# Kernel optimization log

Hardware: AMD Instinct MI355X
Metric: run time of the kernel (lower is better)

The kernel has to match this reference:

```python
import jax, jax.numpy as jnp
import numpy as np

B, S, IN, HID = 128, 512, 1024, 1024
CHI, KAPPA, DT = 0.638, 0.35, 0.01
NC = 6  # num zeta corridors


def setup_inputs() -> dict:
    key = jax.random.key(0)
    ks = jax.random.split(key, 10)
    def rn(k, shp, s=0.02):
        return jax.random.normal(k, shp, dtype=jnp.float32) * s
    return {
        "x": jax.random.normal(ks[0], (B, S, IN), dtype=jnp.float32),
        "W_gates": rn(ks[1], (IN + HID, 4 * HID)),  # fused [i|f|g|o] gate weights
        "b_gates": jnp.zeros((4 * HID,), jnp.float32),
        "mirror_W": rn(ks[2], (HID, HID)),
        "mirror_b": jnp.zeros((HID,), jnp.float32),
        "curv_W1": rn(ks[3], (HID, HID // 2)),
        "curv_b1": jnp.zeros((HID // 2,), jnp.float32),
        "curv_W2": rn(ks[4], (HID // 2, 1)),
        "curv_b2": jnp.zeros((1,), jnp.float32),
        "evo_W": rn(ks[5], (HID, HID)),
        "evo_b": jnp.zeros((HID,), jnp.float32),
        "zeta_w": jax.random.normal(ks[6], (NC,), dtype=jnp.float32),
        "zeta_p": jax.random.normal(ks[7], (NC,), dtype=jnp.float32),
    }


def _zeta_loss(zw, zp):
    # Per recurrent step seq_len==1 so s-points are (sigma=0.5, t=-2) for every batch
    # element; the functional-equation loss is therefore a single scalar independent
    # of the hidden state, and the mean over identical points equals that scalar.
    L = 0.2 + 0.1 * jnp.arange(NC, dtype=jnp.float32)  # corridor lengths
    s0 = jnp.complex64(0.5 - 2.0j)
    def xi(s):
        t1 = jnp.exp(-s * L)
        t2 = jax.nn.sigmoid(zp).astype(jnp.complex64) * jnp.exp(-(1.0 - s) * L)
        return jnp.sum(jax.nn.sigmoid(zw).astype(jnp.complex64) * 0.5 * (t1 + t2))
    d = xi(s0) - xi(1.0 - s0)
    return (d * jnp.conj(d)).real  # |Xi(s) - Xi(1-s)|^2


def reference(x, W_gates, b_gates, mirror_W, mirror_b,
              curv_W1, curv_b1, curv_W2, curv_b2,
              evo_W, evo_b, zeta_w, zeta_p):
    Wx, Wh = W_gates[:IN], W_gates[IN:]
    # Precompute the input contribution of all 4 gates for every timestep (one big GEMM).
    gx = jnp.einsum('bsi,ig->bsg', x, Wx) + b_gates        # [B,S,4H]
    gx = jnp.swapaxes(gx, 0, 1)                            # [S,B,4H] for scan
    h0 = jnp.zeros((x.shape[0], HID), x.dtype)
    c0 = jnp.zeros((x.shape[0], HID), x.dtype)

    def step(carry, g):
        h, c = carry
        gates = g + h @ Wh                                  # [B,4H]
        i, f, gg, o = jnp.split(gates, 4, axis=-1)
        i, f, o = jax.nn.sigmoid(i), jax.nn.sigmoid(f), jax.nn.sigmoid(o)
        gg = jnp.tanh(gg)
        c = f * c + i * gg
        # curvature coupling: scalar curvature per batch element gates an evolution step
        kap = CHI * (jax.nn.relu(c @ curv_W1 + curv_b1) @ curv_W2 + curv_b2)  # [B,1]
        c = c + DT * kap * (c @ evo_W + evo_b)
        # mirror operator + guardian threshold
        h = jnp.tanh((o * jnp.tanh(c)) @ mirror_W + mirror_b)
        h = h / (1.0 + KAPPA * jnp.abs(h))
        return (h, c), h

    (h, c), ys = jax.lax.scan(step, (h0, c0), gx)
    outputs = jnp.swapaxes(ys, 0, 1)                        # [B,S,H]
    # zeta regularization loss is identical each step, so the seq-mean equals one eval
    return outputs, h, c, _zeta_loss(zeta_w, zeta_p)
```

## Files before the change

### kernel.cpp

```cpp
#include <hip/hip_runtime.h>
#include <hip/hip_bf16.h>
#include <math.h>
#include <stdint.h>

#define B_    128
#define S_    512
#define IN_   1024
#define HID_  1024
#define CHI_  0.638f
#define KAPPA_ 0.35f
#define DT_   0.01f
#define CH    32
#define NCHUNK (S_/CH)

#define OUT_H 67108864
#define OUT_C 67239936
#define OUT_Z 67371008

#define WS_CNT   0
#define WS_KP    2048
#define WS_HBF   6144
#define WS_CF32  268288
#define WS_STATE_BYTES 792576
#define WS_CBF   792576
#define WS_MBF   1054720
#define WS_WGT   1316864
#define WS_EVOT  18094080
#define WS_MIRT  20191232
#define WS_C1T   22288384
#define WS_XBF   23336960
#define WS_GXC   31725568

using s16x8 = __attribute__((ext_vector_type(8))) short;
using s16x4 = __attribute__((ext_vector_type(4))) short;
using f32x4 = __attribute__((ext_vector_type(4))) float;
typedef unsigned long long u64;

static __device__ __forceinline__ short f2bf(float x){
  unsigned int u = __float_as_uint(x);
  u = (u + 0x7FFFu + ((u >> 16) & 1u)) >> 16;
  return (short)u;
}
static __device__ __forceinline__ float b2f(short s){
  return __uint_as_float(((unsigned int)(unsigned short)s) << 16);
}
static __device__ __forceinline__ float sigf(float x){
  return 1.f / (1.f + __expf(-x));
}
static __device__ __forceinline__ float tanhf_(float x){
  return 1.f - 2.f / (__expf(2.f * x) + 1.f);
}
static __device__ __forceinline__ f32x4 mfma16(s16x8 a, s16x8 b, f32x4 c){
  return __builtin_amdgcn_mfma_f32_16x16x32_bf16(a, b, c, 0, 0, 0);
}

static __device__ __forceinline__ u64 ld_coh_u64(const void* p){
  return __hip_atomic_load((const u64*)p, __ATOMIC_RELAXED, __HIP_MEMORY_SCOPE_AGENT);
}
static __device__ __forceinline__ void st_coh_u64(void* p, u64 v){
  __hip_atomic_store((u64*)p, v, __ATOMIC_RELAXED, __HIP_MEMORY_SCOPE_AGENT);
}
static __device__ __forceinline__ float ld_coh_f32(const float* p){
  return __hip_atomic_load(p, __ATOMIC_RELAXED, __HIP_MEMORY_SCOPE_AGENT);
}
static __device__ __forceinline__ void st_coh_f32(float* p, float v){
  __hip_atomic_store(p, v, __ATOMIC_RELAXED, __HIP_MEMORY_SCOPE_AGENT);
}
static __device__ __forceinline__ unsigned ld_coh_u32(const unsigned* p){
  return __hip_atomic_load(p, __ATOMIC_RELAXED, __HIP_MEMORY_SCOPE_AGENT);
}
static __device__ __forceinline__ void st_coh_u32(unsigned* p, unsigned v){
  __hip_atomic_store(p, v, __ATOMIC_RELAXED, __HIP_MEMORY_SCOPE_AGENT);
}
static __device__ __forceinline__ void at_add_f32(float* p, float v){
  __hip_atomic_fetch_add(p, v, __ATOMIC_RELAXED, __HIP_MEMORY_SCOPE_AGENT);
}
static __device__ __forceinline__ s16x8 ld_coh16B(const short* p){
  union { u64 q[2]; s16x8 v; } u;
  u.q[0] = ld_coh_u64(p);
  u.q[1] = ld_coh_u64(p + 4);
  return u.v;
}

static __device__ __forceinline__ void gbar(unsigned* arr, int n, unsigned gen){
  asm volatile("s_waitcnt vmcnt(0)" ::: "memory");
  __syncthreads();
  if (threadIdx.x < 32){
    if (threadIdx.x == 0) st_coh_u32(arr + n, gen);
    unsigned v = ld_coh_u32(arr + threadIdx.x);
    while (!__all(v >= gen)){
      __builtin_amdgcn_s_sleep(2);
      v = ld_coh_u32(arr + threadIdx.x);
    }
  }
  __syncthreads();
}

__global__ void transpose_bf(const float* __restrict__ in, short* __restrict__ out,
                             int R, int C){
  __shared__ float tile[32][33];
  int c0 = blockIdx.x * 32, r0 = blockIdx.y * 32;
  int tc = threadIdx.x & 31, tr = threadIdx.x >> 5;
  #pragma unroll
  for (int i = 0; i < 4; i++){
    int r = tr + i * 8;
    tile[r][tc] = in[(size_t)(r0 + r) * C + (c0 + tc)];
  }
  __syncthreads();
  #pragma unroll
  for (int i = 0; i < 4; i++){
    int cc = tr + i * 8;
    out[(size_t)(c0 + cc) * R + (r0 + tc)] = f2bf(tile[tc][cc]);
  }
}

__global__ void conv_x(const float* __restrict__ x, short* __restrict__ xbf, int t0){
  int rb = blockIdx.x;
  int tl = rb >> 7, b = rb & 127;
  const float* src = x + ((size_t)b * S_ + (t0 + tl)) * (size_t)IN_;
  short* dst = xbf + (size_t)rb * IN_;
  int i = threadIdx.x * 4;
  float4 v = *(const float4*)(src + i);
  s16x4 o; o[0]=f2bf(v.x); o[1]=f2bf(v.y); o[2]=f2bf(v.z); o[3]=f2bf(v.w);
  *(s16x4*)(dst + i) = o;
}

__global__ __launch_bounds__(256, 2) void gemm_gx(const short* __restrict__ Ax,
                                                  const short* __restrict__ wgT,
                                                  short* __restrict__ gxc){
  __shared__ short As[128 * 32];
  __shared__ short Bs[128 * 32];
  const int tid = threadIdx.x, w = tid >> 6, l = tid & 63;
  const int wm = w & 1, wn = w >> 1;
  const int bn = blockIdx.x, bm = blockIdx.y;
  const int lc = l & 15, kg = l >> 4;
  f32x4 acc[4][4];
  #pragma unroll
  for (int i = 0; i < 4; i++)
    #pragma unroll
    for (int j = 0; j < 4; j++) acc[i][j] = f32x4{0.f, 0.f, 0.f, 0.f};

  const int srow = tid >> 1;
  const int so = (tid & 1) * 32;
  const short* ga = Ax  + (size_t)(bm * 128 + srow) * 1024 + (so >> 1);
  const short* gb = wgT + (size_t)(bn * 128 + srow) * 2048 + (so >> 1);
  const int sp0 = srow * 64 + ((so)      ^ ((srow & 3) << 4));
  const int sp1 = srow * 64 + ((so + 16) ^ ((srow & 3) << 4));

  uint4 ra0, ra1, rb0, rb1;
  auto LD = [&](int kt){
    ra0 = *(const uint4*)(ga + kt * 32);
    ra1 = *(const uint4*)(ga + kt * 32 + 8);
    rb0 = *(const uint4*)(gb + kt * 32);
    rb1 = *(const uint4*)(gb + kt * 32 + 8);
  };
  LD(0);
  for (int kt = 0; kt < 32; ++kt){
    __syncthreads();
    *(uint4*)((char*)As + sp0) = ra0;
    *(uint4*)((char*)As + sp1) = ra1;
    *(uint4*)((char*)Bs + sp0) = rb0;
    *(uint4*)((char*)Bs + sp1) = rb1;
    __syncthreads();
    if (kt + 1 < 32) LD(kt + 1);
    s16x8 af[4], bfr[4];
    #pragma unroll
    for (int mf = 0; mf < 4; ++mf){
      int row = wm * 64 + mf * 16 + lc;
      af[mf] = *(const s16x8*)((const char*)As + row * 64 + ((kg * 16) ^ ((row & 3) << 4)));
    }
    #pragma unroll
    for (int nf = 0; nf < 4; ++nf){
      int row = wn * 64 + nf * 16 + lc;
      bfr[nf] = *(const s16x8*)((const char*)Bs + row * 64 + ((kg * 16) ^ ((row & 3) << 4)));
    }
    #pragma unroll
    for (int mf = 0; mf < 4; ++mf)
      #pragma unroll
      for (int nf = 0; nf < 4; ++nf)
        acc[mf][nf] = mfma16(af[mf], bfr[nf], acc[mf][nf]);
  }
  #pragma unroll
  for (int mf = 0; mf < 4; ++mf){
    #pragma unroll
    for (int nf = 0; nf < 4; ++nf){
      int gg = wm * 4 + mf;
      int gc = bn * 128 + wn * 64 + nf * 16 + lc;
      s16x4 pk;
      #pragma unroll
      for (int r = 0; r < 4; r++) pk[r] = f2bf(acc[mf][nf][r]);
      *(s16x4*)(gxc + (((size_t)bm * 8 + gg) * 4096 + gc) * 16 + kg * 4) = pk;
    }
  }
}

struct cpx { double r, i; };
static __device__ cpx cexp_(cpx z){ double e = exp(z.r); return {e * cos(z.i), e * sin(z.i)}; }
static __device__ cpx xi_(double sr, double si, const float* zw, const float* zp){
  cpx acc{0.0, 0.0};
  for (int i = 0; i < 6; i++){
    double L = 0.2 + 0.1 * i;
    double sw = 1.0 / (1.0 + exp(-(double)zw[i]));
    double sp = 1.0 / (1.0 + exp(-(double)zp[i]));
    cpx t1 = cexp_({-sr * L, -si * L});
    cpx t2 = cexp_({-(1.0 - sr) * L, si * L});
    acc.r += sw * 0.5 * (t1.r + sp * t2.r);
    acc.i += sw * 0.5 * (t1.i + sp * t2.i);
  }
  return acc;
}
__global__ void zeta_k(const float* __restrict__ zw, const float* __restrict__ zp,
                       float* __restrict__ dz){
  if (threadIdx.x == 0 && blockIdx.x == 0){
    cpx a = xi_(0.5, -2.0, zw, zp);
    cpx b = xi_(0.5,  2.0, zw, zp);
    double dr = a.r - b.r, di = a.i - b.i;
    dz[0] = (float)(dr * dr + di * di);
  }
}

#define RSLOT(slot, j) ((char*)red + (slot) * 8192 + (size_t)l * 128 + (((j) * 16) ^ ((l & 7) << 4)))

__global__ __launch_bounds__(512, 2) void scan_k(
    const short* __restrict__ wgT, const short* __restrict__ evoT,
    const short* __restrict__ mirT, const short* __restrict__ c1T,
    const short* __restrict__ gxc,
    const float* __restrict__ bg,  const float* __restrict__ evob,
    const float* __restrict__ mirb, const float* __restrict__ cb1,
    const float* __restrict__ cw2, const float* __restrict__ cb2,
    short* __restrict__ hbf, short* __restrict__ cbf, short* __restrict__ mbf,
    float* __restrict__ cf32, float* __restrict__ kp,
    unsigned int* __restrict__ cnt, float* __restrict__ dout, int t0)
{
  const int tid = threadIdx.x;
  const int w = tid >> 6, l = tid & 63;
  const int lc = l & 15, kg = l >> 4;
  const int bi = blockIdx.x;
  const int g = bi >> 5, n = bi & 31;
  unsigned* arr = cnt + g * 64;

  __shared__ float red[4][64][32];
  __shared__ float gatesL[4][16][33];
  __shared__ float eL[16][33];
  __shared__ float kpart[16][8];
  __shared__ float kapL[16];
  __shared__ short stL[16][32];
  __shared__ float hfL[16][32];

  const short* hG = hbf + (size_t)g * 16384;
  const short* cG = cbf + (size_t)g * 16384;
  const short* mG = mbf + (size_t)g * 16384;
  float* kpg = kp + g * 128;

  const int pl = (tid & 127) >> 1, ph = tid & 1;
  const size_t poff = (size_t)(n * 64 + pl) * 8 + ph * 4;
  const int psr = pl & 15, psc = (pl >> 4) * 8 + ph * 4;

  const int orow = tid >> 5, ocolL = tid & 31;
  const int ocol = n * 32 + ocolL;
  const size_t oidx = (size_t)(g * 16 + orow) * HID_ + ocol;
  float c_state = cf32[oidx];
  float o_reg = 0.f;
  float bgv[4];
  #pragma unroll
  for (int q = 0; q < 4; q++) bgv[q] = bg[q * 1024 + ocol];
  const float cb2v = cb2[0];

  const short* bqp[4][2];
  #pragma unroll
  for (int q = 0; q < 4; q++)
    #pragma unroll
    for (int cf = 0; cf < 2; cf++)
      bqp[q][cf] = wgT + (size_t)(q * 1024 + n * 32 + cf * 16 + lc) * 2048 + 1024 + w * 128 + kg * 8;
  const short* bevo0 = evoT + (size_t)(n * 32 + lc) * 1024 + w * 128 + kg * 8;
  const short* bevo1 = bevo0 + 16 * 1024;
  const short* bcur  = c1T + (size_t)(n * 16 + lc) * 1024 + w * 128 + kg * 8;
  const short* bmir0 = mirT + (size_t)(n * 32 + lc) * 1024 + w * 128 + kg * 8;
  const short* bmir1 = bmir0 + 16 * 1024;
  const float eb0 = evob[n * 32 + lc], eb1 = evob[n * 32 + 16 + lc];
  const float c1bv = cb1[n * 16 + lc], c2wv = cw2[n * 16 + lc];
  const float mb0 = mirb[n * 32 + lc], mb1 = mirb[n * 32 + 16 + lc];

  unsigned gen = (unsigned)t0 * 4;

  for (int lt = 0; lt < CH; ++lt){
    const int t = t0 + lt;

    float gxv[4];
    #pragma unroll
    for (int q = 0; q < 4; q++)
      gxv[q] = b2f(gxc[(((size_t)lt * 8 + g) * 4096 + q * 1024 + ocol) * 16 + orow]);

    {
      f32x4 acc[4][2];
      #pragma unroll
      for (int q = 0; q < 4; q++){ acc[q][0] = f32x4{0,0,0,0}; acc[q][1] = f32x4{0,0,0,0}; }
      #pragma unroll
      for (int ks = 0; ks < 4; ++ks){
        int kq = w * 4 + ks;
        s16x8 a = ld_coh16B(hG + (size_t)(kq * 64 + l) * 8);
        #pragma unroll
        for (int q = 0; q < 4; q++){
          s16x8 b0 = *(const s16x8*)(bqp[q][0] + ks * 32);
          s16x8 b1 = *(const s16x8*)(bqp[q][1] + ks * 32);
          acc[q][0] = mfma16(a, b0, acc[q][0]);
          acc[q][1] = mfma16(a, b1, acc[q][1]);
        }
      }
      f32x4* accf = (f32x4*)acc;
      if (w >= 4){
        #pragma unroll
        for (int j = 0; j < 8; j++) *(f32x4*)RSLOT(w - 4, j) = accf[j];
      }
      __syncthreads();
      if (w < 4){
        #pragma unroll
        for (int j = 0; j < 8; j++) accf[j] += *(const f32x4*)RSLOT(w, j);
      }
      __syncthreads();
      if (w == 2 || w == 3){
        #pragma unroll
        for (int j = 0; j < 8; j++) *(f32x4*)RSLOT(w - 2, j) = accf[j];
      }
      __syncthreads();
      if (w < 2){
        #pragma unroll
        for (int j = 0; j < 8; j++) accf[j] += *(const f32x4*)RSLOT(w, j);
      }
      __syncthreads();
      if (w == 1){
        #pragma unroll
        for (int j = 0; j < 8; j++) *(f32x4*)RSLOT(0, j) = accf[j];
      }
      __syncthreads();
      if (w == 0){
        #pragma unroll
        for (int j = 0; j < 8; j++) accf[j] += *(const f32x4*)RSLOT(0, j);
        #pragma unroll
        for (int q = 0; q < 4; q++)
          #pragma unroll
          for (int cf = 0; cf < 2; cf++)
            #pragma unroll
            for (int r = 0; r < 4; r++)
              gatesL[q][kg * 4 + r][cf * 16 + lc] = acc[q][cf][r];
      }
      __syncthreads();
      float pre[4];
      #pragma unroll
      for (int q = 0; q < 4; q++)
        pre[q] = gatesL[q][orow][ocolL] + bgv[q] + gxv[q];
      float ii = sigf(pre[0]), ff = sigf(pre[1]);
      float gt = tanhf_(pre[2]);
      o_reg = sigf(pre[3]);
      c_state = ff * c_state + ii * gt;
      stL[orow][ocolL] = f2bf(c_state);
      __syncthreads();
      if (tid < 128)
        st_coh_u64((void*)(cG + poff), *(const u64*)&stL[psr][psc]);
    }
    gbar(arr, n, ++gen);

    {
      f32x4 e0{0,0,0,0}, e1{0,0,0,0}, cv{0,0,0,0};
      #pragma unroll
      for (int ks = 0; ks < 4; ++ks){
        int kq = w * 4 + ks;
        s16x8 a = ld_coh16B(cG + (size_t)(kq * 64 + l) * 8);
        s16x8 b0 = *(const s16x8*)(bevo0 + ks * 32);
        s16x8 b1 = *(const s16x8*)(bevo1 + ks * 32);
        s16x8 bc = *(const s16x8*)(bcur + ks * 32);
        e0 = mfma16(a, b0, e0);
        e1 = mfma16(a, b1, e1);
        cv = mfma16(a, bc, cv);
      }
      if (w >= 4){
        *(f32x4*)RSLOT(w - 4, 0) = e0; *(f32x4*)RSLOT(w - 4, 1) = e1; *(f32x4*)RSLOT(w - 4, 2) = cv;
      }
      __syncthreads();
      if (w < 4){
        e0 += *(const f32x4*)RSLOT(w, 0); e1 += *(const f32x4*)RSLOT(w, 1); cv += *(const f32x4*)RSLOT(w, 2);
      }
      __syncthreads();
      if (w == 2 || w == 3){
        *(f32x4*)RSLOT(w - 2, 0) = e0; *(f32x4*)RSLOT(w - 2, 1) = e1; *(f32x4*)RSLOT(w - 2, 2) = cv;
      }
      __syncthreads();
      if (w < 2){
        e0 += *(const f32x4*)RSLOT(w, 0); e1 += *(const f32x4*)RSLOT(w, 1); cv += *(const f32x4*)RSLOT(w, 2);
      }
      __syncthreads();
      if (w == 1){
        *(f32x4*)RSLOT(0, 0) = e0; *(f32x4*)RSLOT(0, 1) = e1; *(f32x4*)RSLOT(0, 2) = cv;
      }
      __syncthreads();
      if (w == 0){
        e0 += *(const f32x4*)RSLOT(0, 0); e1 += *(const f32x4*)RSLOT(0, 1); cv += *(const f32x4*)RSLOT(0, 2);
        #pragma unroll
        for (int r = 0; r < 4; r++){
          eL[kg * 4 + r][lc]      = e0[r] + eb0;
          eL[kg * 4 + r][16 + lc] = e1[r] + eb1;
          float v = fmaxf(cv[r] + c1bv, 0.f) * c2wv;
          v += __shfl_xor(v, 1); v += __shfl_xor(v, 2);
          v += __shfl_xor(v, 4); v += __shfl_xor(v, 8);
          if (lc == 0)
            at_add_f32(kpg + (kg * 4 + r) * 8 + (n >> 2), v);
        }
      }
    }
    gbar(arr, n, ++gen);

    {
      if (tid < 128)
        kpart[tid >> 3][tid & 7] = ld_coh_f32(kpg + tid);
      __syncthreads();
      if (tid < 16){
        float s = 0.f;
        #pragma unroll
        for (int j = 0; j < 8; j++) s += kpart[tid][j];
        kapL[tid] = CHI_ * (s + cb2v);
      }
      __syncthreads();
      {
        float e = eL[orow][ocolL];
        c_state = c_state + DT_ * kapL[orow] * e;
        float mm = o_reg * tanhf_(c_state);
        stL[orow][ocolL] = f2bf(mm);
        if (t == S_ - 1) dout[OUT_C + oidx] = c_state;
        if (lt == CH - 1) cf32[oidx] = c_state;
      }
      __syncthreads();
      if (tid < 128)
        st_coh_u64((void*)(mG + poff), *(const u64*)&stL[psr][psc]);
    }
    gbar(arr, n, ++gen);

    {
      f32x4 h0{0,0,0,0}, h1{0,0,0,0};
      #pragma unroll
      for (int ks = 0; ks < 4; ++ks){
        int kq = w * 4 + ks;
        s16x8 a = ld_coh16B(mG + (size_t)(kq * 64 + l) * 8);
        s16x8 b0 = *(const s16x8*)(bmir0 + ks * 32);
        s16x8 b1 = *(const s16x8*)(bmir1 + ks * 32);
        h0 = mfma16(a, b0, h0);
        h1 = mfma16(a, b1, h1);
      }
      if (w >= 4){ *(f32x4*)RSLOT(w - 4, 0) = h0; *(f32x4*)RSLOT(w - 4, 1) = h1; }
      __syncthreads();
      if (w < 4){ h0 += *(const f32x4*)RSLOT(w, 0); h1 += *(const f32x4*)RSLOT(w, 1); }
      __syncthreads();
      if (w == 2 || w == 3){ *(f32x4*)RSLOT(w - 2, 0) = h0; *(f32x4*)RSLOT(w - 2, 1) = h1; }
      __syncthreads();
      if (w < 2){ h0 += *(const f32x4*)RSLOT(w, 0); h1 += *(const f32x4*)RSLOT(w, 1); }
      __syncthreads();
      if (w == 1){ *(f32x4*)RSLOT(0, 0) = h0; *(f32x4*)RSLOT(0, 1) = h1; }
      __syncthreads();
      if (w == 0){
        h0 += *(const f32x4*)RSLOT(0, 0); h1 += *(const f32x4*)RSLOT(0, 1);
        #pragma unroll
        for (int cf = 0; cf < 2; cf++){
          #pragma unroll
          for (int r = 0; r < 4; r++){
            int row = kg * 4 + r;
            float hv = tanhf_((cf ? h1[r] : h0[r]) + (cf ? mb1 : mb0));
            hv = hv / (1.f + KAPPA_ * fabsf(hv));
            hfL[row][cf * 16 + lc] = hv;
            stL[row][cf * 16 + lc] = f2bf(hv);
          }
        }
      }
      __syncthreads();
      {
        float hv = hfL[orow][ocolL];
        dout[(size_t)(g * 16 + orow) * 524288 + (size_t)t * 1024 + ocol] = hv;
        if (t == S_ - 1) dout[OUT_H + oidx] = hv;
      }
      if (tid < 128)
        st_coh_u64((void*)(hG + poff), *(const u64*)&stL[psr][psc]);
      if (n == 0 && tid >= 128 && tid < 256)
        st_coh_f32(kpg + (tid - 128), 0.f);
    }
    gbar(arr, n, ++gen);
  }
}

extern "C" void kernel_launch(void* const* d_in, const int* in_sizes, int n_in,
                              void* d_out, int out_size, void* d_ws, size_t ws_size,
                              hipStream_t stream)
{
  (void)in_sizes; (void)n_in; (void)out_size; (void)ws_size;
  const float* x   = (const float*)d_in[0];
  const float* Wg  = (const float*)d_in[1];
  const float* bg  = (const float*)d_in[2];
  const float* miW = (const float*)d_in[3];
  const float* mib = (const float*)d_in[4];
  const float* c1W = (const float*)d_in[5];
  const float* c1b = (const float*)d_in[6];
  const float* c2W = (const float*)d_in[7];
  const float* c2b = (const float*)d_in[8];
  const float* evW = (const float*)d_in[9];
  const float* evb = (const float*)d_in[10];
  const float* zw  = (const float*)d_in[11];
  const float* zp  = (const float*)d_in[12];
  float* out = (float*)d_out;
  char* ws = (char*)d_ws;

  unsigned int* cnt = (unsigned int*)(ws + WS_CNT);
  float* kpb  = (float*)(ws + WS_KP);
  short* hbf  = (short*)(ws + WS_HBF);
  float* cf32 = (float*)(ws + WS_CF32);
  short* cbf  = (short*)(ws + WS_CBF);
  short* mbf  = (short*)(ws + WS_MBF);
  short* wgT  = (short*)(ws + WS_WGT);
  short* evoT = (short*)(ws + WS_EVOT);
  short* mirT = (short*)(ws + WS_MIRT);
  short* c1T  = (short*)(ws + WS_C1T);
  short* xbf  = (short*)(ws + WS_XBF);
  short* gxc  = (short*)(ws + WS_GXC);

  hipMemsetAsync(ws, 0, WS_STATE_BYTES, stream);

  transpose_bf<<<dim3(4096/32, 2048/32), 256, 0, stream>>>(Wg,  wgT, 2048, 4096);
  transpose_bf<<<dim3(1024/32, 1024/32), 256, 0, stream>>>(evW, evoT, 1024, 1024);
  transpose_bf<<<dim3(1024/32, 1024/32), 256, 0, stream>>>(miW, mirT, 1024, 1024);
  transpose_bf<<<dim3(512/32, 1024/32),  256, 0, stream>>>(c1W, c1T, 1024, 512);

  zeta_k<<<1, 64, 0, stream>>>(zw, zp, out + OUT_Z);

  for (int ch = 0; ch < NCHUNK; ++ch){
    conv_x<<<dim3(CH * 128), 256, 0, stream>>>(x, xbf, ch * CH);
    gemm_gx<<<dim3(32, CH), 256, 0, stream>>>(xbf, wgT, gxc);
    scan_k<<<dim3(256), 512, 0, stream>>>(wgT, evoT, mirT, c1T, gxc,
                                          bg, evb, mib, c1b, c2W, c2b,
                                          hbf, cbf, mbf, cf32, kpb,
                                          cnt, out, ch * CH);
  }
}
```

Baseline: 11.95 ms.

## Stage shared A operand in LDS and split waves by output tile instead of K

Each recurrent phase now loads the full 16x1024 bf16 activation tile for the group into LDS once, using coherent global loads, and then has each wave compute a distinct output tile across the whole K dimension. This replaces the earlier K-split across 8 waves, which needed a multi-round LDS tree reduction with several __syncthreads per phase. The change removes those reduction barriers and the per-wave coherent A loads. In exchange, the evo/curv and mirror phases use only 2-3 of the 8 waves, each running a longer serial MFMA chain, so latency on the critical path may rise.

```diff
diff --git a/kernel.cpp b/kernel.cpp
--- a/kernel.cpp
+++ b/kernel.cpp
@@ -74,12 +74,6 @@
 }
 static __device__ __forceinline__ void at_add_f32(float* p, float v){
   __hip_atomic_fetch_add(p, v, __ATOMIC_RELAXED, __HIP_MEMORY_SCOPE_AGENT);
-}
-static __device__ __forceinline__ s16x8 ld_coh16B(const short* p){
-  union { u64 q[2]; s16x8 v; } u;
-  u.q[0] = ld_coh_u64(p);
-  u.q[1] = ld_coh_u64(p + 4);
-  return u.v;
 }
 
 static __device__ __forceinline__ void gbar(unsigned* arr, int n, unsigned gen){
@@ -219,8 +213,6 @@
   }
 }
 
-#define RSLOT(slot, j) ((char*)red + (slot) * 8192 + (size_t)l * 128 + (((j) * 16) ^ ((l & 7) << 4)))
-
 __global__ __launch_bounds__(512, 2) void scan_k(
     const short* __restrict__ wgT, const short* __restrict__ evoT,
     const short* __restrict__ mirT, const short* __restrict__ c1T,
@@ -239,7 +231,7 @@
   const int g = bi >> 5, n = bi & 31;
   unsigned* arr = cnt + g * 64;
 
-  __shared__ float red[4][64][32];
+  __shared__ short aS[16384];
   __shared__ float gatesL[4][16][33];
   __shared__ float eL[16][33];
   __shared__ float kpart[16][8];
@@ -251,6 +243,24 @@
   const short* cG = cbf + (size_t)g * 16384;
   const short* mG = mbf + (size_t)g * 16384;
   float* kpg = kp + g * 128;
+
+  auto stage = [&](const short* G){
+    const short* p = G + tid * 8;
+    s16x8 v0, v1, v2, v3;
+    asm volatile(
+      "global_load_dwordx4 %0, %4, off sc0 sc1\n\t"
+      "global_load_dwordx4 %1, %5, off sc0 sc1\n\t"
+      "global_load_dwordx4 %2, %6, off sc0 sc1\n\t"
+      "global_load_dwordx4 %3, %7, off sc0 sc1\n\t"
+      "s_waitcnt vmcnt(0)"
+      : "=&v"(v0), "=&v"(v1), "=&v"(v2), "=&v"(v3)
+      : "v"(p), "v"(p + 4096), "v"(p + 8192), "v"(p + 12288)
+      : "memory");
+    *(s16x8*)(aS + tid * 8)         = v0;
+    *(s16x8*)(aS + tid * 8 + 4096)  = v1;
+    *(s16x8*)(aS + tid * 8 + 8192)  = v2;
+    *(s16x8*)(aS + tid * 8 + 12288) = v3;
+  };
 
   const int pl = (tid & 127) >> 1, ph = tid & 1;
   const size_t poff = (size_t)(n * 64 + pl) * 8 + ph * 4;
@@ -266,20 +276,12 @@
   for (int q = 0; q < 4; q++) bgv[q] = bg[q * 1024 + ocol];
   const float cb2v = cb2[0];
 
-  const short* bqp[4][2];
-  #pragma unroll
-  for (int q = 0; q < 4; q++)
-    #pragma unroll
-    for (int cf = 0; cf < 2; cf++)
-      bqp[q][cf] = wgT + (size_t)(q * 1024 + n * 32 + cf * 16 + lc) * 2048 + 1024 + w * 128 + kg * 8;
-  const short* bevo0 = evoT + (size_t)(n * 32 + lc) * 1024 + w * 128 + kg * 8;
-  const short* bevo1 = bevo0 + 16 * 1024;
-  const short* bcur  = c1T + (size_t)(n * 16 + lc) * 1024 + w * 128 + kg * 8;
-  const short* bmir0 = mirT + (size_t)(n * 32 + lc) * 1024 + w * 128 + kg * 8;
-  const short* bmir1 = bmir0 + 16 * 1024;
-  const float eb0 = evob[n * 32 + lc], eb1 = evob[n * 32 + 16 + lc];
+  const int qA = w >> 1, cfA = w & 1;
+  const short* bA = wgT + (size_t)(qA * 1024 + n * 32 + cfA * 16 + lc) * 2048 + 1024 + kg * 8;
+  const short* bB = evoT + (size_t)(n * 32 + (w & 1) * 16 + lc) * 1024 + kg * 8;
+  const short* bC = c1T + (size_t)(n * 16 + lc) * 1024 + kg * 8;
+  const short* bD = mirT + (size_t)(n * 32 + (w & 1) * 16 + lc) * 1024 + kg * 8;
   const float c1bv = cb1[n * 16 + lc], c2wv = cw2[n * 16 + lc];
-  const float mb0 = mirb[n * 32 + lc], mb1 = mirb[n * 32 + 16 + lc];
 
   unsigned gen = (unsigned)t0 * 4;
 
@@ -292,58 +294,18 @@
       gxv[q] = b2f(gxc[(((size_t)lt * 8 + g) * 4096 + q * 1024 + ocol) * 16 + orow]);
 
     {
-      f32x4 acc[4][2];
+      stage(hG);
+      __syncthreads();
+      f32x4 acc{0.f, 0.f, 0.f, 0.f};
       #pragma unroll
-      for (int q = 0; q < 4; q++){ acc[q][0] = f32x4{0,0,0,0}; acc[q][1] = f32x4{0,0,0,0}; }
+      for (int kq = 0; kq < 32; ++kq){
+        s16x8 a = *(const s16x8*)(aS + (kq * 64 + l) * 8);
+        s16x8 b = *(const s16x8*)(bA + kq * 32);
+        acc = mfma16(a, b, acc);
+      }
       #pragma unroll
-      for (int ks = 0; ks < 4; ++ks){
-        int kq = w * 4 + ks;
-        s16x8 a = ld_coh16B(hG + (size_t)(kq * 64 + l) * 8);
-        #pragma unroll
-        for (int q = 0; q < 4; q++){
-          s16x8 b0 = *(const s16x8*)(bqp[q][0] + ks * 32);
-          s16x8 b1 = *(const s16x8*)(bqp[q][1] + ks * 32);
-          acc[q][0] = mfma16(a, b0, acc[q][0]);
-          acc[q][1] = mfma16(a, b1, acc[q][1]);
-        }
-      }
-      f32x4* accf = (f32x4*)acc;
-      if (w >= 4){
-        #pragma unroll
-        for (int j = 0; j < 8; j++) *(f32x4*)RSLOT(w - 4, j) = accf[j];
-      }
-      __syncthreads();
-      if (w < 4){
-        #pragma unroll
-        for (int j = 0; j < 8; j++) accf[j] += *(const f32x4*)RSLOT(w, j);
-      }
-      __syncthreads();
-      if (w == 2 || w == 3){
-        #pragma unroll
-        for (int j = 0; j < 8; j++) *(f32x4*)RSLOT(w - 2, j) = accf[j];
-      }
-      __syncthreads();
-      if (w < 2){
-        #pragma unroll
-        for (int j = 0; j < 8; j++) accf[j] += *(const f32x4*)RSLOT(w, j);
-      }
-      __syncthreads();
-      if (w == 1){
-        #pragma unroll
-        for (int j = 0; j < 8; j++) *(f32x4*)RSLOT(0, j) = accf[j];
-      }
-      __syncthreads();
-      if (w == 0){
-        #pragma unroll
-        for (int j = 0; j < 8; j++) accf[j] += *(const f32x4*)RSLOT(0, j);
-        #pragma unroll
-        for (int q = 0; q < 4; q++)
-          #pragma unroll
-          for (int cf = 0; cf < 2; cf++)
-            #pragma unroll
-            for (int r = 0; r < 4; r++)
-              gatesL[q][kg * 4 + r][cf * 16 + lc] = acc[q][cf][r];
-      }
+      for (int r = 0; r < 4; r++)
+        gatesL[qA][kg * 4 + r][cfA * 16 + lc] = acc[r];
       __syncthreads();
       float pre[4];
       #pragma unroll
@@ -361,45 +323,31 @@
     gbar(arr, n, ++gen);
 
     {
-      f32x4 e0{0,0,0,0}, e1{0,0,0,0}, cv{0,0,0,0};
-      #pragma unroll
-      for (int ks = 0; ks < 4; ++ks){
-        int kq = w * 4 + ks;
-        s16x8 a = ld_coh16B(cG + (size_t)(kq * 64 + l) * 8);
-        s16x8 b0 = *(const s16x8*)(bevo0 + ks * 32);
-        s16x8 b1 = *(const s16x8*)(bevo1 + ks * 32);
-        s16x8 bc = *(const s16x8*)(bcur + ks * 32);
-        e0 = mfma16(a, b0, e0);
-        e1 = mfma16(a, b1, e1);
-        cv = mfma16(a, bc, cv);
-      }
-      if (w >= 4){
-        *(f32x4*)RSLOT(w - 4, 0) = e0; *(f32x4*)RSLOT(w - 4, 1) = e1; *(f32x4*)RSLOT(w - 4, 2) = cv;
-      }
-      __syncthreads();
-      if (w < 4){
-        e0 += *(const f32x4*)RSLOT(w, 0); e1 += *(const f32x4*)RSLOT(w, 1); cv += *(const f32x4*)RSLOT(w, 2);
-      }
-      __syncthreads();
-      if (w == 2 || w == 3){
-        *(f32x4*)RSLOT(w - 2, 0) = e0; *(f32x4*)RSLOT(w - 2, 1) = e1; *(f32x4*)RSLOT(w - 2, 2) = cv;
-      }
+      stage(cG);
       __syncthreads();
       if (w < 2){
-        e0 += *(const f32x4*)RSLOT(w, 0); e1 += *(const f32x4*)RSLOT(w, 1); cv += *(const f32x4*)RSLOT(w, 2);
-      }
-      __syncthreads();
-      if (w == 1){
-        *(f32x4*)RSLOT(0, 0) = e0; *(f32x4*)RSLOT(0, 1) = e1; *(f32x4*)RSLOT(0, 2) = cv;
-      }
-      __syncthreads();
-      if (w == 0){
-        e0 += *(const f32x4*)RSLOT(0, 0); e1 += *(const f32x4*)RSLOT(0, 1); cv += *(const f32x4*)RSLOT(0, 2);
+        f32x4 acc{0.f, 0.f, 0.f, 0.f};
+        #pragma unroll
+        for (int kq = 0; kq < 32; ++kq){
+          s16x8 a = *(const s16x8*)(aS + (kq * 64 + l) * 8);
+          s16x8 b = *(const s16x8*)(bB + kq * 32);
+          acc = mfma16(a, b, acc);
+        }
+        float eb = evob[n * 32 + w * 16 + lc];
+        #pragma unroll
+        for (int r = 0; r < 4; r++)
+          eL[kg * 4 + r][w * 16 + lc] = acc[r] + eb;
+      } else if (w == 2){
+        f32x4 acc{0.f, 0.f, 0.f, 0.f};
+        #pragma unroll
+        for (int kq = 0; kq < 32; ++kq){
+          s16x8 a = *(const s16x8*)(aS + (kq * 64 + l) * 8);
+          s16x8 b = *(const s16x8*)(bC + kq * 32);
+          acc = mfma16(a, b, acc);
+        }
         #pragma unroll
         for (int r = 0; r < 4; r++){
-          eL[kg * 4 + r][lc]      = e0[r] + eb0;
-          eL[kg * 4 + r][16 + lc] = e1[r] + eb1;
-          float v = fmaxf(cv[r] + c1bv, 0.f) * c2wv;
+          float v = fmaxf(acc[r] + c1bv, 0.f) * c2wv;
           v += __shfl_xor(v, 1); v += __shfl_xor(v, 2);
           v += __shfl_xor(v, 4); v += __shfl_xor(v, 8);
           if (lc == 0)
@@ -435,38 +383,24 @@
     gbar(arr, n, ++gen);
 
     {
-      f32x4 h0{0,0,0,0}, h1{0,0,0,0};
-      #pragma unroll
-      for (int ks = 0; ks < 4; ++ks){
-        int kq = w * 4 + ks;
-        s16x8 a = ld_coh16B(mG + (size_t)(kq * 64 + l) * 8);
-        s16x8 b0 = *(const s16x8*)(bmir0 + ks * 32);
-        s16x8 b1 = *(const s16x8*)(bmir1 + ks * 32);
-        h0 = mfma16(a, b0, h0);
-        h1 = mfma16(a, b1, h1);
-      }
-      if (w >= 4){ *(f32x4*)RSLOT(w - 4, 0) = h0; *(f32x4*)RSLOT(w - 4, 1) = h1; }
-      __syncthreads();
-      if (w < 4){ h0 += *(const f32x4*)RSLOT(w, 0); h1 += *(const f32x4*)RSLOT(w, 1); }
-      __syncthreads();
-      if (w == 2 || w == 3){ *(f32x4*)RSLOT(w - 2, 0) = h0; *(f32x4*)RSLOT(w - 2, 1) = h1; }
-      __syncthreads();
-      if (w < 2){ h0 += *(const f32x4*)RSLOT(w, 0); h1 += *(const f32x4*)RSLOT(w, 1); }
-      __syncthreads();
-      if (w == 1){ *(f32x4*)RSLOT(0, 0) = h0; *(f32x4*)RSLOT(0, 1) = h1; }
-      __syncthreads();
-      if (w == 0){
-        h0 += *(const f32x4*)RSLOT(0, 0); h1 += *(const f32x4*)RSLOT(0, 1);
-        #pragma unroll
-        for (int cf = 0; cf < 2; cf++){
-          #pragma unroll
-          for (int r = 0; r < 4; r++){
-            int row = kg * 4 + r;
-            float hv = tanhf_((cf ? h1[r] : h0[r]) + (cf ? mb1 : mb0));
-            hv = hv / (1.f + KAPPA_ * fabsf(hv));
-            hfL[row][cf * 16 + lc] = hv;
-            stL[row][cf * 16 + lc] = f2bf(hv);
-          }
+      stage(mG);
+      __syncthreads();
+      if (w < 2){
+        f32x4 acc{0.f, 0.f, 0.f, 0.f};
+        #pragma unroll
+        for (int kq = 0; kq < 32; ++kq){
+          s16x8 a = *(const s16x8*)(aS + (kq * 64 + l) * 8);
+          s16x8 b = *(const s16x8*)(bD + kq * 32);
+          acc = mfma16(a, b, acc);
+        }
+        float mb = mirb[n * 32 + w * 16 + lc];
+        #pragma unroll
+        for (int r = 0; r < 4; r++){
+          int row = kg * 4 + r;
+          float hv = tanhf_(acc[r] + mb);
+          hv = hv / (1.f + KAPPA_ * fabsf(hv));
+          hfL[row][w * 16 + lc] = hv;
+          stL[row][w * 16 + lc] = f2bf(hv);
         }
       }
       __syncthreads();
```

Measured after the change: 17.22 ms. 1.44x slower.

## Remove one grid barrier per step by recomputing mirror input from shared c, e, o

Applied to the files above, without the earlier changes.

Each recurrent step drops its third grid-group barrier. The gate stage now publishes o (bf16) and the evolution stage publishes e (bf16). The mirror GEMM then rebuilds o*tanh(c + DT*kap*e) on the fly from the shared c, e and o buffers instead of waiting for a separately published m buffer. The curvature partial-sum buffer is double-buffered by step parity so it can be zeroed without the removed barrier. This trades extra global loads and transcendental work per MFMA operand, plus extra bf16 rounding of e and o, for one fewer cross-block synchronisation per timestep.

```diff
diff --git a/kernel.cpp b/kernel.cpp
--- a/kernel.cpp
+++ b/kernel.cpp
@@ -19,17 +19,18 @@
 
 #define WS_CNT   0
 #define WS_KP    2048
-#define WS_HBF   6144
-#define WS_CF32  268288
-#define WS_STATE_BYTES 792576
-#define WS_CBF   792576
-#define WS_MBF   1054720
-#define WS_WGT   1316864
-#define WS_EVOT  18094080
-#define WS_MIRT  20191232
-#define WS_C1T   22288384
-#define WS_XBF   23336960
-#define WS_GXC   31725568
+#define WS_HBF   10240
+#define WS_CF32  272384
+#define WS_STATE_BYTES 796672
+#define WS_CBF   796672
+#define WS_OBF   1058816
+#define WS_EBF   1320960
+#define WS_WGT   1583104
+#define WS_EVOT  18360320
+#define WS_MIRT  20457472
+#define WS_C1T   22554624
+#define WS_XBF   23603200
+#define WS_GXC   31991808
 
 using s16x8 = __attribute__((ext_vector_type(8))) short;
 using s16x4 = __attribute__((ext_vector_type(4))) short;
@@ -228,8 +229,8 @@
     const float* __restrict__ bg,  const float* __restrict__ evob,
     const float* __restrict__ mirb, const float* __restrict__ cb1,
     const float* __restrict__ cw2, const float* __restrict__ cb2,
-    short* __restrict__ hbf, short* __restrict__ cbf, short* __restrict__ mbf,
-    float* __restrict__ cf32, float* __restrict__ kp,
+    short* __restrict__ hbf, short* __restrict__ cbf, short* __restrict__ obf,
+    short* __restrict__ ebf, float* __restrict__ cf32, float* __restrict__ kp,
     unsigned int* __restrict__ cnt, float* __restrict__ dout, int t0)
 {
   const int tid = threadIdx.x;
@@ -245,12 +246,14 @@
   __shared__ float kpart[16][8];
   __shared__ float kapL[16];
   __shared__ short stL[16][32];
+  __shared__ short oSt[16][32];
   __shared__ float hfL[16][32];
 
   const short* hG = hbf + (size_t)g * 16384;
   const short* cG = cbf + (size_t)g * 16384;
-  const short* mG = mbf + (size_t)g * 16384;
-  float* kpg = kp + g * 128;
+  const short* oG = obf + (size_t)g * 16384;
+  const short* eG = ebf + (size_t)g * 16384;
+  float* kpg = kp + g * 256;
 
   const int pl = (tid & 127) >> 1, ph = tid & 1;
   const size_t poff = (size_t)(n * 64 + pl) * 8 + ph * 4;
@@ -260,7 +263,6 @@
   const int ocol = n * 32 + ocolL;
   const size_t oidx = (size_t)(g * 16 + orow) * HID_ + ocol;
   float c_state = cf32[oidx];
-  float o_reg = 0.f;
   float bgv[4];
   #pragma unroll
   for (int q = 0; q < 4; q++) bgv[q] = bg[q * 1024 + ocol];
@@ -281,10 +283,11 @@
   const float c1bv = cb1[n * 16 + lc], c2wv = cw2[n * 16 + lc];
   const float mb0 = mirb[n * 32 + lc], mb1 = mirb[n * 32 + 16 + lc];
 
-  unsigned gen = (unsigned)t0 * 4;
+  unsigned gen = (unsigned)t0 * 3;
 
   for (int lt = 0; lt < CH; ++lt){
     const int t = t0 + lt;
+    const int par = lt & 1;
 
     float gxv[4];
     #pragma unroll
@@ -351,12 +354,16 @@
         pre[q] = gatesL[q][orow][ocolL] + bgv[q] + gxv[q];
       float ii = sigf(pre[0]), ff = sigf(pre[1]);
       float gt = tanhf_(pre[2]);
-      o_reg = sigf(pre[3]);
+      float oo = sigf(pre[3]);
       c_state = ff * c_state + ii * gt;
       stL[orow][ocolL] = f2bf(c_state);
-      __syncthreads();
-      if (tid < 128)
-        st_coh_u64((void*)(cG + poff), *(const u64*)&stL[psr][psc]);
+      oSt[orow][ocolL] = f2bf(oo);
+      __syncthreads();
+      if (tid < 256){
+        short* dst = (short*)((tid < 128 ? cG : oG) + poff);
+        const short* src = (tid < 128 ? &stL[psr][psc] : &oSt[psr][psc]);
+        st_coh_u64(dst, *(const u64*)src);
+      }
     }
     gbar(arr, n, ++gen);
 
@@ -403,15 +410,22 @@
           v += __shfl_xor(v, 1); v += __shfl_xor(v, 2);
           v += __shfl_xor(v, 4); v += __shfl_xor(v, 8);
           if (lc == 0)
-            at_add_f32(kpg + (kg * 4 + r) * 8 + (n >> 2), v);
+            at_add_f32(kpg + par * 128 + (kg * 4 + r) * 8 + (n >> 2), v);
         }
+      }
+      __syncthreads();
+      if (tid < 128){
+        union { u64 q; short s[4]; } up;
+        #pragma unroll
+        for (int j = 0; j < 4; j++) up.s[j] = f2bf(eL[psr][psc + j]);
+        st_coh_u64((void*)(eG + poff), up.q);
       }
     }
     gbar(arr, n, ++gen);
 
     {
       if (tid < 128)
-        kpart[tid >> 3][tid & 7] = ld_coh_f32(kpg + tid);
+        kpart[tid >> 3][tid & 7] = ld_coh_f32(kpg + par * 128 + tid);
       __syncthreads();
       if (tid < 16){
         float s = 0.f;
@@ -423,27 +437,25 @@
       {
         float e = eL[orow][ocolL];
         c_state = c_state + DT_ * kapL[orow] * e;
-        float mm = o_reg * tanhf_(c_state);
-        stL[orow][ocolL] = f2bf(mm);
         if (t == S_ - 1) dout[OUT_C + oidx] = c_state;
         if (lt == CH - 1) cf32[oidx] = c_state;
       }
-      __syncthreads();
-      if (tid < 128)
-        st_coh_u64((void*)(mG + poff), *(const u64*)&stL[psr][psc]);
-    }
-    gbar(arr, n, ++gen);
-
-    {
+      const float kap_l = kapL[lc];
       f32x4 h0{0,0,0,0}, h1{0,0,0,0};
       #pragma unroll
       for (int ks = 0; ks < 4; ++ks){
-        int kq = w * 4 + ks;
-        s16x8 a = ld_coh16B(mG + (size_t)(kq * 64 + l) * 8);
+        const size_t off = (size_t)((w * 4 + ks) * 64 + l) * 8;
+        s16x8 cf = ld_coh16B(cG + off);
+        s16x8 ef = ld_coh16B(eG + off);
+        s16x8 of = ld_coh16B(oG + off);
+        s16x8 m;
+        #pragma unroll
+        for (int j = 0; j < 8; j++)
+          m[j] = f2bf(b2f(of[j]) * tanhf_(b2f(cf[j]) + DT_ * kap_l * b2f(ef[j])));
         s16x8 b0 = *(const s16x8*)(bmir0 + ks * 32);
         s16x8 b1 = *(const s16x8*)(bmir1 + ks * 32);
-        h0 = mfma16(a, b0, h0);
-        h1 = mfma16(a, b1, h1);
+        h0 = mfma16(m, b0, h0);
+        h1 = mfma16(m, b1, h1);
       }
       if (w >= 4){ *(f32x4*)RSLOT(w - 4, 0) = h0; *(f32x4*)RSLOT(w - 4, 1) = h1; }
       __syncthreads();
@@ -478,7 +490,7 @@
       if (tid < 128)
         st_coh_u64((void*)(hG + poff), *(const u64*)&stL[psr][psc]);
       if (n == 0 && tid >= 128 && tid < 256)
-        st_coh_f32(kpg + (tid - 128), 0.f);
+        st_coh_f32(kpg + (par ^ 1) * 128 + (tid - 128), 0.f);
     }
     gbar(arr, n, ++gen);
   }
@@ -510,7 +522,8 @@
   short* hbf  = (short*)(ws + WS_HBF);
   float* cf32 = (float*)(ws + WS_CF32);
   short* cbf  = (short*)(ws + WS_CBF);
-  short* mbf  = (short*)(ws + WS_MBF);
+  short* obf  = (short*)(ws + WS_OBF);
+  short* ebf  = (short*)(ws + WS_EBF);
   short* wgT  = (short*)(ws + WS_WGT);
   short* evoT = (short*)(ws + WS_EVOT);
   short* mirT = (short*)(ws + WS_MIRT);
@@ -532,7 +545,7 @@
     gemm_gx<<<dim3(32, CH), 256, 0, stream>>>(xbf, wgT, gxc);
     scan_k<<<dim3(256), 512, 0, stream>>>(wgT, evoT, mirT, c1T, gxc,
                                           bg, evb, mib, c1b, c2W, c2b,
-                                          hbf, cbf, mbf, cf32, kpb,
+                                          hbf, cbf, obf, ebf, cf32, kpb,
                                           cnt, out, ch * CH);
   }
 }
```

New measurement: 12.63 ms. +5.7%, slower.

## Overlap next-chunk input GEMM with recurrent scan via fused launch and double buffering

Applied to the files above, without the earlier changes.

Extra blocks are appended to the persistent scan kernel launch. They compute the next chunk's input-gate GEMM into a second gx buffer while the scan blocks process the current chunk. This is meant to hide the separate per-chunk GEMM launch and its runtime behind the latency-bound recurrence. The fused path only runs when the workspace is large enough for the second buffer; otherwise the old sequential path is kept. Costs: the GEMM blocks now run with 512-thread blocks, half of them idle, under the scan kernel's register budget. They may also compete with the barrier-synchronised scan blocks for CU slots and memory bandwidth.

```diff
diff --git a/kernel.cpp b/kernel.cpp
--- a/kernel.cpp
+++ b/kernel.cpp
@@ -30,6 +30,8 @@
 #define WS_C1T   22288384
 #define WS_XBF   23336960
 #define WS_GXC   31725568
+#define WS_GXC2  65280000
+#define WS_NEED_FUSED 98834432ull
 
 using s16x8 = __attribute__((ext_vector_type(8))) short;
 using s16x4 = __attribute__((ext_vector_type(4))) short;
@@ -125,14 +127,15 @@
   *(s16x4*)(dst + i) = o;
 }
 
-__global__ __launch_bounds__(256, 2) void gemm_gx(const short* __restrict__ Ax,
-                                                  const short* __restrict__ wgT,
-                                                  short* __restrict__ gxc){
-  __shared__ short As[128 * 32];
-  __shared__ short Bs[128 * 32];
-  const int tid = threadIdx.x, w = tid >> 6, l = tid & 63;
+static __device__ void gemm_body(const short* __restrict__ Ax,
+                                 const short* __restrict__ wgT,
+                                 short* __restrict__ gxc, int bid,
+                                 short* As, short* Bs){
+  const int tid = threadIdx.x;
+  if (tid >= 256) return;
+  const int w = tid >> 6, l = tid & 63;
   const int wm = w & 1, wn = w >> 1;
-  const int bn = blockIdx.x, bm = blockIdx.y;
+  const int bn = bid & 31, bm = bid >> 5;
   const int lc = l & 15, kg = l >> 4;
   f32x4 acc[4][4];
   #pragma unroll
@@ -194,6 +197,14 @@
   }
 }
 
+__global__ __launch_bounds__(256, 2) void gemm_gx(const short* __restrict__ Ax,
+                                                  const short* __restrict__ wgT,
+                                                  short* __restrict__ gxc){
+  __shared__ short As[128 * 32];
+  __shared__ short Bs[128 * 32];
+  gemm_body(Ax, wgT, gxc, blockIdx.x + blockIdx.y * 32, As, Bs);
+}
+
 struct cpx { double r, i; };
 static __device__ cpx cexp_(cpx z){ double e = exp(z.r); return {e * cos(z.i), e * sin(z.i)}; }
 static __device__ cpx xi_(double sr, double si, const float* zw, const float* zp){
@@ -230,22 +241,41 @@
     const float* __restrict__ cw2, const float* __restrict__ cb2,
     short* __restrict__ hbf, short* __restrict__ cbf, short* __restrict__ mbf,
     float* __restrict__ cf32, float* __restrict__ kp,
-    unsigned int* __restrict__ cnt, float* __restrict__ dout, int t0)
+    unsigned int* __restrict__ cnt, float* __restrict__ dout, int t0,
+    const short* __restrict__ xbfN, short* __restrict__ gxcW)
 {
+  __shared__ union ShU {
+    struct {
+      float red[4][64][32];
+      float gatesL[4][16][33];
+      float eL[16][33];
+      float kpart[16][8];
+      float kapL[16];
+      short stL[16][32];
+      float hfL[16][32];
+    } s;
+    struct { short As[128 * 32]; short Bs[128 * 32]; } gm;
+  } sh;
+
+  const int bi = blockIdx.x;
+  if (bi >= 256){
+    gemm_body(xbfN, wgT, gxcW, bi - 256, sh.gm.As, sh.gm.Bs);
+    return;
+  }
+
   const int tid = threadIdx.x;
   const int w = tid >> 6, l = tid & 63;
   const int lc = l & 15, kg = l >> 4;
-  const int bi = blockIdx.x;
   const int g = bi >> 5, n = bi & 31;
   unsigned* arr = cnt + g * 64;
 
-  __shared__ float red[4][64][32];
-  __shared__ float gatesL[4][16][33];
-  __shared__ float eL[16][33];
-  __shared__ float kpart[16][8];
-  __shared__ float kapL[16];
-  __shared__ short stL[16][32];
-  __shared__ float hfL[16][32];
+  float (&red)[4][64][32]   = sh.s.red;
+  float (&gatesL)[4][16][33] = sh.s.gatesL;
+  float (&eL)[16][33]       = sh.s.eL;
+  float (&kpart)[16][8]     = sh.s.kpart;
+  float (&kapL)[16]         = sh.s.kapL;
+  short (&stL)[16][32]      = sh.s.stL;
+  float (&hfL)[16][32]      = sh.s.hfL;
 
   const short* hG = hbf + (size_t)g * 16384;
   const short* cG = cbf + (size_t)g * 16384;
@@ -488,7 +518,7 @@
                               void* d_out, int out_size, void* d_ws, size_t ws_size,
                               hipStream_t stream)
 {
-  (void)in_sizes; (void)n_in; (void)out_size; (void)ws_size;
+  (void)in_sizes; (void)n_in; (void)out_size;
   const float* x   = (const float*)d_in[0];
   const float* Wg  = (const float*)d_in[1];
   const float* bg  = (const float*)d_in[2];
@@ -516,7 +546,9 @@
   short* mirT = (short*)(ws + WS_MIRT);
   short* c1T  = (short*)(ws + WS_C1T);
   short* xbf  = (short*)(ws + WS_XBF);
-  short* gxc  = (short*)(ws + WS_GXC);
+  short* gxc0 = (short*)(ws + WS_GXC);
+  const bool fused = (ws_size >= WS_NEED_FUSED);
+  short* gxc1 = fused ? (short*)(ws + WS_GXC2) : gxc0;
 
   hipMemsetAsync(ws, 0, WS_STATE_BYTES, stream);
 
@@ -527,12 +559,28 @@
 
   zeta_k<<<1, 64, 0, stream>>>(zw, zp, out + OUT_Z);
 
+  conv_x<<<dim3(CH * 128), 256, 0, stream>>>(x, xbf, 0);
+  gemm_gx<<<dim3(32, CH), 256, 0, stream>>>(xbf, wgT, gxc0);
+
   for (int ch = 0; ch < NCHUNK; ++ch){
-    conv_x<<<dim3(CH * 128), 256, 0, stream>>>(x, xbf, ch * CH);
-    gemm_gx<<<dim3(32, CH), 256, 0, stream>>>(xbf, wgT, gxc);
-    scan_k<<<dim3(256), 512, 0, stream>>>(wgT, evoT, mirT, c1T, gxc,
-                                          bg, evb, mib, c1b, c2W, c2b,
-                                          hbf, cbf, mbf, cf32, kpb,
-                                          cnt, out, ch * CH);
-  }
-}
+    const bool hasNext = (ch + 1 < NCHUNK);
+    short* gxR = (ch & 1) ? gxc1 : gxc0;
+    short* gxW = ((ch + 1) & 1) ? gxc1 : gxc0;
+    if (hasNext)
+      conv_x<<<dim3(CH * 128), 256, 0, stream>>>(x, xbf, (ch + 1) * CH);
+    if (fused){
+      int nb = hasNext ? (256 + 1024) : 256;
+      scan_k<<<dim3(nb), 512, 0, stream>>>(wgT, evoT, mirT, c1T, gxR,
+                                           bg, evb, mib, c1b, c2W, c2b,
+                                           hbf, cbf, mbf, cf32, kpb,
+                                           cnt, out, ch * CH, xbf, gxW);
+    } else {
+      scan_k<<<dim3(256), 512, 0, stream>>>(wgT, evoT, mirT, c1T, gxc0,
+                                            bg, evb, mib, c1b, c2W, c2b,
+                                            hbf, cbf, mbf, cf32, kpb,
+                                            cnt, out, ch * CH, xbf, gxc0);
+      if (hasNext)
+        gemm_gx<<<dim3(32, CH), 256, 0, stream>>>(xbf, wgT, gxc0);
+    }
+  }
+}
```

Result: slower. 12.87 ms (+7.6%).
